# Performance work log

Measured on AMD Instinct MI355X. Metric: run time of the kernel, lower is better.

Reference implementation:

```python
import jax, jax.numpy as jnp
import numpy as np

NEG = -9.0e15


def setup_inputs() -> dict:
    key = jax.random.key(0)
    ks = jax.random.split(key, 8)
    N, D_IN, D_OUT, EMB = 100000, 128, 128, 64
    E, NPE = 50000, 32   # hyperedges, nodes per edge
    U, EPN = 50000, 32   # output nodes, edges per node
    stdv = 1.0 / np.sqrt(D_IN)
    return {
        "x": jax.random.normal(ks[0], (N, D_IN), dtype=jnp.float32),
        "seq": jax.random.randint(ks[1], (E, NPE), 0, N, dtype=jnp.int64),
        "text2emb": jax.random.normal(ks[2], (100, EMB), dtype=jnp.float32),
        "useq": jax.random.randint(ks[3], (U, EPN), 0, E, dtype=jnp.int64),
        "data_idx": jax.random.randint(ks[4], (U,), 0, U, dtype=jnp.int64),
        "weight1": jax.random.uniform(ks[5], (D_IN, D_OUT), jnp.float32, -stdv, stdv),
        "weight2": jax.random.uniform(ks[6], (D_OUT, D_OUT), jnp.float32, -stdv, stdv),
        "weight3": jax.random.uniform(ks[7], (100, EMB), jnp.float32, -stdv, stdv),
    }


def _masked_mean_weights(idx):
    # softmax over a {1, -9e15} mask -> uniform weights over nonzero slots
    logits = jnp.where(idx > 0, jnp.float32(1.0), jnp.float32(NEG))
    return jax.nn.softmax(logits, axis=1)


def reference(x, seq, text2emb, useq, data_idx, weight1, weight2, weight3):
    # text_weight is computed in the original forward but never used
    w3n = weight3 / jnp.linalg.norm(weight3, axis=1, keepdims=True)
    cos = w3n @ w3n.T
    _text_weight = cos.mean(axis=1).mean()  # scalar, unused downstream

    h = x @ weight1                              # [N, D_OUT]
    adj_fea = h[seq]                             # [E, NPE, D_OUT] gather
    w = _masked_mean_weights(seq)                # [E, NPE]
    edge = jnp.einsum("enc,en->ec", adj_fea, w)  # [E, D_OUT]
    # dropout is identity in eval mode
    edge = jax.nn.relu(edge)
    e1 = edge @ weight2                          # [E, D_OUT]

    edge_fea = e1[useq]                          # [U, EPN, D_OUT] gather
    uw = _masked_mean_weights(useq)              # [U, EPN]
    node = jnp.einsum("uec,ue->uc", edge_fea, uw)  # [U, D_OUT]
    return node
```

## Files before the change

### kernel.cpp

```cpp
#include <hip/hip_runtime.h>
#include <hip/hip_bf16.h>

#define N_NODES  100000
#define E_EDGES  50000
#define U_NODES  50000
#define D        128
#define NPE      32

typedef __attribute__((ext_vector_type(8))) short short8;
typedef __attribute__((ext_vector_type(4))) unsigned short u16x4;
typedef __attribute__((ext_vector_type(4))) float f32x4;

static __device__ __forceinline__ unsigned short f2bf_bits(float f) {
    unsigned u = __float_as_uint(f);
    return (unsigned short)((u + 0x7fffu + ((u >> 16) & 1u)) >> 16);
}

__global__ void prep_wt(const float* __restrict__ w1, const float* __restrict__ w2,
                        unsigned short* __restrict__ wt) {
    const int t = blockIdx.x * 256 + threadIdx.x;
    const int which = t >> 14;
    const int e = t & 16383;
    const int k = e >> 7, c = e & 127;
    const float* w = which ? w2 : w1;
    wt[which * 16384 + c * 128 + k] = f2bf_bits(w[e]);
}

template<int A_BF16>
__global__ __launch_bounds__(256) void gemm_mfma(const void* __restrict__ Ap,
                                                 const unsigned short* __restrict__ Wt,
                                                 unsigned short* __restrict__ C, int M) {
    __shared__ unsigned short sW[128 * 136];
    __shared__ unsigned short sA[64 * 136];
    __shared__ unsigned short sC[64 * 132];
    const int tid = threadIdx.x;

    {
        const float4* src = (const float4*)Wt;
#pragma unroll
        for (int j = 0; j < 8; ++j) {
            const int i = tid + j * 256;
            const int r = i >> 4, c16 = i & 15;
            *(float4*)&sW[r * 136 + c16 * 8] = src[i];
        }
    }

    const int ntiles = (M + 63) >> 6;
    const int lane = tid & 63;
    const int wv = tid >> 6;
    const int r16 = lane & 15;
    const int hi = lane >> 4;

    float4 pf[8];

    auto load_tile = [&](int tile) {
        const int row0 = tile << 6;
        if (A_BF16) {
            const unsigned short* A = (const unsigned short*)Ap;
#pragma unroll
            for (int j = 0; j < 4; ++j) {
                const int i = tid + j * 256;
                int gr = row0 + (i >> 4); if (gr >= M) gr = M - 1;
                pf[j] = *(const float4*)&A[(size_t)gr * D + (i & 15) * 8];
            }
        } else {
            const float* A = (const float*)Ap;
#pragma unroll
            for (int j = 0; j < 8; ++j) {
                const int i = tid + j * 256;
                int gr = row0 + (i >> 5); if (gr >= M) gr = M - 1;
                pf[j] = *(const float4*)&A[(size_t)gr * D + (i & 31) * 4];
            }
        }
    };
    auto write_tile = [&]() {
        if (A_BF16) {
#pragma unroll
            for (int j = 0; j < 4; ++j) {
                const int i = tid + j * 256;
                *(float4*)&sA[(i >> 4) * 136 + (i & 15) * 8] = pf[j];
            }
        } else {
#pragma unroll
            for (int j = 0; j < 8; ++j) {
                const int i = tid + j * 256;
                const float4 v = pf[j];
                u16x4 p;
                p.x = f2bf_bits(v.x); p.y = f2bf_bits(v.y);
                p.z = f2bf_bits(v.z); p.w = f2bf_bits(v.w);
                *(u16x4*)&sA[(i >> 5) * 136 + (i & 31) * 4] = p;
            }
        }
    };

    int tile = blockIdx.x;
    if (tile >= ntiles) return;
    load_tile(tile);

    while (tile < ntiles) {
        write_tile();
        __syncthreads();

        const int next = tile + gridDim.x;
        if (next < ntiles) load_tile(next);

        short8 af[4];
#pragma unroll
        for (int kt = 0; kt < 4; ++kt)
            af[kt] = *(const short8*)&sA[(wv * 16 + r16) * 136 + kt * 32 + hi * 8];

        f32x4 acc[8];
#pragma unroll
        for (int ct = 0; ct < 8; ++ct) acc[ct] = (f32x4){0.f, 0.f, 0.f, 0.f};
#pragma unroll
        for (int ct = 0; ct < 8; ++ct) {
#pragma unroll
            for (int kt = 0; kt < 4; ++kt) {
                const short8 bf = *(const short8*)&sW[(ct * 16 + r16) * 136 + kt * 32 + hi * 8];
                acc[ct] = __builtin_amdgcn_mfma_f32_16x16x32_bf16(af[kt], bf, acc[ct], 0, 0, 0);
            }
        }
        __syncthreads();

        const int row0 = tile << 6;
        const int nrows = min(64, M - row0);
#pragma unroll
        for (int ct = 0; ct < 8; ++ct)
#pragma unroll
            for (int i = 0; i < 4; ++i)
                sC[(wv * 16 + hi * 4 + i) * 132 + ct * 16 + r16] = f2bf_bits(acc[ct][i]);
        __syncthreads();
#pragma unroll
        for (int j = 0; j < 4; ++j) {
            const int i = tid + j * 256;
            const int r = i >> 4, cc = i & 15;
            if (r < nrows)
                *(float4*)&C[(size_t)(row0 + r) * D + cc * 8] =
                    *(const float4*)&sC[r * 132 + cc * 8];
        }
        tile = next;
    }
}

template<int OUT_BF16, int RELU>
__global__ __launch_bounds__(256) void gather_mean4(
        const unsigned short* __restrict__ src, const int* __restrict__ idx,
        void* __restrict__ dst, int M) {
    const int wid = (int)((blockIdx.x * blockDim.x + threadIdx.x) >> 6);
    if (wid >= M) return;
    const int lane = threadIdx.x & 63;
    const int g = lane >> 4;
    const int c = lane & 15;

    int my = 0;
    if (lane < NPE) my = idx[(size_t)wid * NPE + lane];
    const unsigned long long b = __ballot(lane < NPE && my > 0);
    const int count = __popcll(b);
    const float scale = 1.0f / (float)(count > 0 ? count : NPE);
    const bool take_all = (count == 0);

    uint4 v[8];
    float w[8];
#pragma unroll
    for (int i = 0; i < 8; ++i) {
        const int id = __shfl(my, i * 4 + g);
        w[i] = (take_all || id > 0) ? scale : 0.0f;
        v[i] = *(const uint4*)(src + (size_t)id * D + c * 8);
    }

    float acc[8] = {0.f, 0.f, 0.f, 0.f, 0.f, 0.f, 0.f, 0.f};
#pragma unroll
    for (int i = 0; i < 8; ++i) {
        acc[0] = fmaf(__uint_as_float(v[i].x << 16),         w[i], acc[0]);
        acc[1] = fmaf(__uint_as_float(v[i].x & 0xffff0000u), w[i], acc[1]);
        acc[2] = fmaf(__uint_as_float(v[i].y << 16),         w[i], acc[2]);
        acc[3] = fmaf(__uint_as_float(v[i].y & 0xffff0000u), w[i], acc[3]);
        acc[4] = fmaf(__uint_as_float(v[i].z << 16),         w[i], acc[4]);
        acc[5] = fmaf(__uint_as_float(v[i].z & 0xffff0000u), w[i], acc[5]);
        acc[6] = fmaf(__uint_as_float(v[i].w << 16),         w[i], acc[6]);
        acc[7] = fmaf(__uint_as_float(v[i].w & 0xffff0000u), w[i], acc[7]);
    }

#pragma unroll
    for (int i = 0; i < 8; ++i) {
        acc[i] += __shfl_xor(acc[i], 16);
        acc[i] += __shfl_xor(acc[i], 32);
        if (RELU) acc[i] = fmaxf(acc[i], 0.f);
    }

    if (lane < 16) {
        if (OUT_BF16) {
            uint4 o;
            o.x = (unsigned)f2bf_bits(acc[0]) | ((unsigned)f2bf_bits(acc[1]) << 16);
            o.y = (unsigned)f2bf_bits(acc[2]) | ((unsigned)f2bf_bits(acc[3]) << 16);
            o.z = (unsigned)f2bf_bits(acc[4]) | ((unsigned)f2bf_bits(acc[5]) << 16);
            o.w = (unsigned)f2bf_bits(acc[6]) | ((unsigned)f2bf_bits(acc[7]) << 16);
            *(uint4*)((unsigned short*)dst + (size_t)wid * D + c * 8) = o;
        } else {
            float* dp = (float*)dst + (size_t)wid * D + c * 8;
            *(float4*)dp = make_float4(acc[0], acc[1], acc[2], acc[3]);
            *(float4*)(dp + 4) = make_float4(acc[4], acc[5], acc[6], acc[7]);
        }
    }
}

extern "C" void kernel_launch(void* const* d_in, const int* in_sizes, int n_in,
                              void* d_out, int out_size, void* d_ws, size_t ws_size,
                              hipStream_t stream) {
    const float* x    = (const float*)d_in[0];
    const int*   seq  = (const int*)d_in[1];
    const int*   useq = (const int*)d_in[3];
    const float* w1   = (const float*)d_in[5];
    const float* w2   = (const float*)d_in[6];
    float* out = (float*)d_out;

    unsigned short* wt   = (unsigned short*)d_ws;
    unsigned short* h    = wt + 2 * 16384;
    unsigned short* edge = h + (size_t)N_NODES * D;
    unsigned short* e1   = edge + (size_t)E_EDGES * D;

    prep_wt<<<128, 256, 0, stream>>>(w1, w2, wt);

    gemm_mfma<0><<<512, 256, 0, stream>>>(x, wt, h, N_NODES);

    gather_mean4<1, 1><<<(E_EDGES * 64) / 256, 256, 0, stream>>>(h, seq, edge, E_EDGES);

    gemm_mfma<1><<<512, 256, 0, stream>>>(edge, wt + 16384, e1, E_EDGES);

    gather_mean4<0, 0><<<(U_NODES * 64) / 256, 256, 0, stream>>>(e1, useq, out, U_NODES);
}
```

Before: 220.7 us.

## Gather-mean raw x before W1 and fuse both GEMMs into one kernel

```diff
diff --git a/kernel.cpp b/kernel.cpp
--- a/kernel.cpp
+++ b/kernel.cpp
@@ -26,120 +26,19 @@
     wt[which * 16384 + c * 128 + k] = f2bf_bits(w[e]);
 }
 
-template<int A_BF16>
-__global__ __launch_bounds__(256) void gemm_mfma(const void* __restrict__ Ap,
-                                                 const unsigned short* __restrict__ Wt,
-                                                 unsigned short* __restrict__ C, int M) {
-    __shared__ unsigned short sW[128 * 136];
-    __shared__ unsigned short sA[64 * 136];
-    __shared__ unsigned short sC[64 * 132];
-    const int tid = threadIdx.x;
-
-    {
-        const float4* src = (const float4*)Wt;
-#pragma unroll
-        for (int j = 0; j < 8; ++j) {
-            const int i = tid + j * 256;
-            const int r = i >> 4, c16 = i & 15;
-            *(float4*)&sW[r * 136 + c16 * 8] = src[i];
-        }
-    }
-
-    const int ntiles = (M + 63) >> 6;
-    const int lane = tid & 63;
-    const int wv = tid >> 6;
-    const int r16 = lane & 15;
-    const int hi = lane >> 4;
-
-    float4 pf[8];
-
-    auto load_tile = [&](int tile) {
-        const int row0 = tile << 6;
-        if (A_BF16) {
-            const unsigned short* A = (const unsigned short*)Ap;
-#pragma unroll
-            for (int j = 0; j < 4; ++j) {
-                const int i = tid + j * 256;
-                int gr = row0 + (i >> 4); if (gr >= M) gr = M - 1;
-                pf[j] = *(const float4*)&A[(size_t)gr * D + (i & 15) * 8];
-            }
-        } else {
-            const float* A = (const float*)Ap;
-#pragma unroll
-            for (int j = 0; j < 8; ++j) {
-                const int i = tid + j * 256;
-                int gr = row0 + (i >> 5); if (gr >= M) gr = M - 1;
-                pf[j] = *(const float4*)&A[(size_t)gr * D + (i & 31) * 4];
-            }
-        }
-    };
-    auto write_tile = [&]() {
-        if (A_BF16) {
-#pragma unroll
-            for (int j = 0; j < 4; ++j) {
-                const int i = tid + j * 256;
-                *(float4*)&sA[(i >> 4) * 136 + (i & 15) * 8] = pf[j];
-            }
-        } else {
-#pragma unroll
-            for (int j = 0; j < 8; ++j) {
-                const int i = tid + j * 256;
-                const float4 v = pf[j];
-                u16x4 p;
-                p.x = f2bf_bits(v.x); p.y = f2bf_bits(v.y);
-                p.z = f2bf_bits(v.z); p.w = f2bf_bits(v.w);
-                *(u16x4*)&sA[(i >> 5) * 136 + (i & 31) * 4] = p;
-            }
-        }
-    };
-
-    int tile = blockIdx.x;
-    if (tile >= ntiles) return;
-    load_tile(tile);
-
-    while (tile < ntiles) {
-        write_tile();
-        __syncthreads();
-
-        const int next = tile + gridDim.x;
-        if (next < ntiles) load_tile(next);
-
-        short8 af[4];
-#pragma unroll
-        for (int kt = 0; kt < 4; ++kt)
-            af[kt] = *(const short8*)&sA[(wv * 16 + r16) * 136 + kt * 32 + hi * 8];
-
-        f32x4 acc[8];
-#pragma unroll
-        for (int ct = 0; ct < 8; ++ct) acc[ct] = (f32x4){0.f, 0.f, 0.f, 0.f};
-#pragma unroll
-        for (int ct = 0; ct < 8; ++ct) {
-#pragma unroll
-            for (int kt = 0; kt < 4; ++kt) {
-                const short8 bf = *(const short8*)&sW[(ct * 16 + r16) * 136 + kt * 32 + hi * 8];
-                acc[ct] = __builtin_amdgcn_mfma_f32_16x16x32_bf16(af[kt], bf, acc[ct], 0, 0, 0);
-            }
-        }
-        __syncthreads();
-
-        const int row0 = tile << 6;
-        const int nrows = min(64, M - row0);
-#pragma unroll
-        for (int ct = 0; ct < 8; ++ct)
-#pragma unroll
-            for (int i = 0; i < 4; ++i)
-                sC[(wv * 16 + hi * 4 + i) * 132 + ct * 16 + r16] = f2bf_bits(acc[ct][i]);
-        __syncthreads();
-#pragma unroll
-        for (int j = 0; j < 4; ++j) {
-            const int i = tid + j * 256;
-            const int r = i >> 4, cc = i & 15;
-            if (r < nrows)
-                *(float4*)&C[(size_t)(row0 + r) * D + cc * 8] =
-                    *(const float4*)&sC[r * 132 + cc * 8];
-        }
-        tile = next;
-    }
+__global__ __launch_bounds__(256) void convert_x(const float* __restrict__ x,
+                                                 unsigned short* __restrict__ xb,
+                                                 int n8) {
+    const int i = blockIdx.x * 256 + threadIdx.x;
+    if (i >= n8) return;
+    const float4 a = ((const float4*)x)[2 * i];
+    const float4 b = ((const float4*)x)[2 * i + 1];
+    uint4 o;
+    o.x = (unsigned)f2bf_bits(a.x) | ((unsigned)f2bf_bits(a.y) << 16);
+    o.y = (unsigned)f2bf_bits(a.z) | ((unsigned)f2bf_bits(a.w) << 16);
+    o.z = (unsigned)f2bf_bits(b.x) | ((unsigned)f2bf_bits(b.y) << 16);
+    o.w = (unsigned)f2bf_bits(b.z) | ((unsigned)f2bf_bits(b.w) << 16);
+    ((uint4*)xb)[i] = o;
 }
 
 template<int OUT_BF16, int RELU>
@@ -167,6 +66,7 @@
         w[i] = (take_all || id > 0) ? scale : 0.0f;
         v[i] = *(const uint4*)(src + (size_t)id * D + c * 8);
     }
+    asm volatile("" ::: "memory");
 
     float acc[8] = {0.f, 0.f, 0.f, 0.f, 0.f, 0.f, 0.f, 0.f};
 #pragma unroll
@@ -204,6 +104,119 @@
     }
 }
 
+__global__ __launch_bounds__(256) void gemm12(const unsigned short* __restrict__ gx,
+                                              const unsigned short* __restrict__ Wt,
+                                              unsigned short* __restrict__ e1, int M) {
+    __shared__ unsigned short sW1[128 * 136];
+    __shared__ unsigned short sW2[128 * 136];
+    __shared__ unsigned short sA[64 * 136];
+    const int tid = threadIdx.x;
+
+    {
+        const float4* w4 = (const float4*)Wt;
+#pragma unroll
+        for (int j = 0; j < 8; ++j) {
+            const int i = tid + j * 256;
+            const int r = i >> 4, c16 = i & 15;
+            *(float4*)&sW1[r * 136 + c16 * 8] = w4[i];
+            *(float4*)&sW2[r * 136 + c16 * 8] = w4[2048 + i];
+        }
+    }
+
+    const int ntiles = (M + 63) >> 6;
+    const int lane = tid & 63;
+    const int wv = tid >> 6;
+    const int r16 = lane & 15;
+    const int hi = lane >> 4;
+
+    float4 pf[4];
+    auto load_tile = [&](int tile) {
+        const int row0 = tile << 6;
+#pragma unroll
+        for (int j = 0; j < 4; ++j) {
+            const int i = tid + j * 256;
+            int gr = row0 + (i >> 4); if (gr >= M) gr = M - 1;
+            pf[j] = *(const float4*)&gx[(size_t)gr * D + (i & 15) * 8];
+        }
+    };
+
+    int tile = blockIdx.x;
+    if (tile >= ntiles) return;
+    load_tile(tile);
+
+    while (tile < ntiles) {
+#pragma unroll
+        for (int j = 0; j < 4; ++j) {
+            const int i = tid + j * 256;
+            *(float4*)&sA[(i >> 4) * 136 + (i & 15) * 8] = pf[j];
+        }
+        __syncthreads();
+
+        const int next = tile + gridDim.x;
+        if (next < ntiles) load_tile(next);
+        asm volatile("" ::: "memory");
+
+        short8 af[4];
+#pragma unroll
+        for (int kt = 0; kt < 4; ++kt)
+            af[kt] = *(const short8*)&sA[(wv * 16 + r16) * 136 + kt * 32 + hi * 8];
+
+        f32x4 acc[8];
+#pragma unroll
+        for (int ct = 0; ct < 8; ++ct) acc[ct] = (f32x4){0.f, 0.f, 0.f, 0.f};
+#pragma unroll
+        for (int ct = 0; ct < 8; ++ct)
+#pragma unroll
+            for (int kt = 0; kt < 4; ++kt) {
+                const short8 bf = *(const short8*)&sW1[(ct * 16 + r16) * 136 + kt * 32 + hi * 8];
+                acc[ct] = __builtin_amdgcn_mfma_f32_16x16x32_bf16(af[kt], bf, acc[ct], 0, 0, 0);
+            }
+
+#pragma unroll
+        for (int ct = 0; ct < 8; ++ct)
+#pragma unroll
+            for (int i = 0; i < 4; ++i)
+                sA[(wv * 16 + hi * 4 + i) * 136 + ct * 16 + r16] =
+                    f2bf_bits(fmaxf(acc[ct][i], 0.f));
+
+        short8 af2[4];
+#pragma unroll
+        for (int kt = 0; kt < 4; ++kt)
+            af2[kt] = *(const short8*)&sA[(wv * 16 + r16) * 136 + kt * 32 + hi * 8];
+
+        f32x4 acc2[8];
+#pragma unroll
+        for (int ct = 0; ct < 8; ++ct) acc2[ct] = (f32x4){0.f, 0.f, 0.f, 0.f};
+#pragma unroll
+        for (int ct = 0; ct < 8; ++ct)
+#pragma unroll
+            for (int kt = 0; kt < 4; ++kt) {
+                const short8 bf = *(const short8*)&sW2[(ct * 16 + r16) * 136 + kt * 32 + hi * 8];
+                acc2[ct] = __builtin_amdgcn_mfma_f32_16x16x32_bf16(af2[kt], bf, acc2[ct], 0, 0, 0);
+            }
+
+#pragma unroll
+        for (int ct = 0; ct < 8; ++ct)
+#pragma unroll
+            for (int i = 0; i < 4; ++i)
+                sA[(wv * 16 + hi * 4 + i) * 136 + ct * 16 + r16] = f2bf_bits(acc2[ct][i]);
+        __syncthreads();
+
+        const int row0 = tile << 6;
+        const int nrows = min(64, M - row0);
+#pragma unroll
+        for (int j = 0; j < 4; ++j) {
+            const int i = tid + j * 256;
+            const int r = i >> 4, cc = i & 15;
+            if (r < nrows)
+                *(float4*)&e1[(size_t)(row0 + r) * D + cc * 8] =
+                    *(const float4*)&sA[r * 136 + cc * 8];
+        }
+        __syncthreads();
+        tile = next;
+    }
+}
+
 extern "C" void kernel_launch(void* const* d_in, const int* in_sizes, int n_in,
                               void* d_out, int out_size, void* d_ws, size_t ws_size,
                               hipStream_t stream) {
@@ -214,18 +227,17 @@
     const float* w2   = (const float*)d_in[6];
     float* out = (float*)d_out;
 
-    unsigned short* wt   = (unsigned short*)d_ws;
-    unsigned short* h    = wt + 2 * 16384;
-    unsigned short* edge = h + (size_t)N_NODES * D;
-    unsigned short* e1   = edge + (size_t)E_EDGES * D;
+    unsigned short* wt = (unsigned short*)d_ws;
+    unsigned short* xb = wt + 2 * 16384;
+    unsigned short* gx = xb + (size_t)N_NODES * D;
+    unsigned short* e1 = gx + (size_t)E_EDGES * D;
 
     prep_wt<<<128, 256, 0, stream>>>(w1, w2, wt);
-
-    gemm_mfma<0><<<512, 256, 0, stream>>>(x, wt, h, N_NODES);
-
-    gather_mean4<1, 1><<<(E_EDGES * 64) / 256, 256, 0, stream>>>(h, seq, edge, E_EDGES);
-
-    gemm_mfma<1><<<512, 256, 0, stream>>>(edge, wt + 16384, e1, E_EDGES);
+    convert_x<<<(N_NODES * D / 8 + 255) / 256, 256, 0, stream>>>(x, xb, N_NODES * D / 8);
+
+    gather_mean4<1, 0><<<(E_EDGES * 64) / 256, 256, 0, stream>>>(xb, seq, gx, E_EDGES);
+
+    gemm12<<<512, 256, 0, stream>>>(gx, wt, e1, E_EDGES);
 
     gather_mean4<0, 0><<<(U_NODES * 64) / 256, 256, 0, stream>>>(e1, useq, out, U_NODES);
 }
```

Result: slower. 232.6 us (+5.4%).
